# Optimization experiments

Hardware: AMD Instinct MI355X
Metric: run time of the kernel (lower is better)

The kernel has to match this reference:

```python
import jax, jax.numpy as jnp
import numpy as np

MIN_, MAX_, KSZ, IGNORE_IDX = 10, 10, 3, -255
B, H, W = 256, 256, 256
LI_MAX_ITERS = 64


def setup_inputs() -> dict:
    key = jax.random.key(0)
    x = jax.random.uniform(key, (B, 1, H, W), dtype=jnp.float32)
    return {"x": x}


def _otsu(hist):
    # hist: [256] counts. Returns Otsu threshold (bin value); fg = img > t.
    bins = jnp.arange(256, dtype=jnp.float32)
    w0 = jnp.cumsum(hist)[:-1]
    w1 = hist.sum() - w0
    s0 = jnp.cumsum(hist * bins)[:-1]
    s_tot = (hist * bins).sum()
    m0 = s0 / jnp.maximum(w0, 1e-12)
    m1 = (s_tot - s0) / jnp.maximum(w1, 1e-12)
    var_b = w0 * w1 * (m0 - m1) ** 2
    return jnp.argmax(var_b).astype(jnp.float32)


def _li(hist, init_t):
    # Histogram-based Li iterative minimum cross-entropy threshold
    # (skimage.filters.threshold_li with initial_guess=init_t).
    bins = jnp.arange(256, dtype=jnp.float32)
    img_min = jnp.min(jnp.where(hist > 0, bins, 255.0))
    vals = bins - img_min  # shift so values >= 0 (as skimage does)
    csum = jnp.cumsum(hist)
    cvsum = jnp.cumsum(hist * vals)
    n_tot, s_tot = csum[-1], cvsum[-1]
    tol = 0.5  # integer image -> half the minimal value spacing

    def body(state):
        t_curr, _, i = state
        # background: img <= t_curr + img_min
        idx = jnp.clip(jnp.floor(t_curr + img_min).astype(jnp.int32), 0, 255)
        n_back, s_back = csum[idx], cvsum[idx]
        n_fore, s_fore = n_tot - n_back, s_tot - s_back
        mean_back = jnp.where(n_back > 0, s_back / jnp.maximum(n_back, 1.0), 0.0)
        mean_fore = s_fore / jnp.maximum(n_fore, 1.0)
        eps = 1e-12
        t_next = (mean_back - mean_fore) / (
            jnp.log(jnp.maximum(mean_back, eps)) - jnp.log(jnp.maximum(mean_fore, eps)))
        t_next = jnp.where(mean_back < eps, mean_fore / 2.0, t_next)
        return (t_next, t_curr, i + 1)

    def cond(state):
        t_curr, t_prev, i = state
        return (jnp.abs(t_curr - t_prev) > tol) & (i < LI_MAX_ITERS)

    t0 = init_t - img_min
    t_fin, _, _ = jax.lax.while_loop(cond, body, (t0, t0 + 10.0, 0))
    return t_fin + img_min


def _sample_mask(key, region, k):
    # Uniform sampling without replacement of up to k pixels from region
    # (bool [H,W]) via random-score top-k (equiv. to torch.multinomial
    # with uniform probs, w/o replacement).
    flat = region.reshape(-1)
    scores = jnp.where(flat, jax.random.uniform(key, (flat.shape[0],)), -1.0)
    top, idx = jax.lax.top_k(scores, k)
    valid = (top >= 0.0).astype(jnp.int32)
    mask = jnp.zeros(flat.shape[0], jnp.int32).at[idx].max(valid)
    return mask.reshape(region.shape)


def _dilate(m):
    # kornia dilation with ones (KSZ,KSZ) kernel on a 0/1 mask == max filter.
    return jax.lax.reduce_window(m, 0, jax.lax.max, (KSZ, KSZ), (1, 1), "SAME")


def _per_image(img_u8, key_fg, key_bg):
    # img_u8: [H,W] int32 in [0,255]
    hist = jnp.zeros(256, jnp.float32).at[img_u8.ravel()].add(1.0)
    otsu = jnp.clip(_otsu(hist), 1.0, 254.0)  # clamp 0->1, 255->254
    li_t = _li(hist, otsu)
    roi = img_u8.astype(jnp.float32) > li_t

    fg = _sample_mask(key_fg, roi, MAX_)
    bg = _sample_mask(key_bg, jnp.logical_not(roi), MIN_)
    if KSZ > 1:
        fg = _dilate(fg)
        bg = _dilate(bg)

    overlap = (fg + bg) == 2
    fg = jnp.where(overlap, 0, fg)
    bg = jnp.where(overlap, 0, bg)

    seeds = jnp.full((H, W), IGNORE_IDX, jnp.int32)
    seeds = jnp.where(bg == 1, 0, seeds)
    seeds = jnp.where(fg == 1, 1, seeds)
    return seeds


def reference(x):
    b = x.shape[0]
    # (cam*255).astype(uint8): truncation, cam in [0,1]
    img = jnp.clip(jnp.floor(x[:, 0] * 255.0), 0, 255).astype(jnp.int32)
    keys = jax.random.split(jax.random.key(1), (b, 2))
    return jax.vmap(_per_image)(img, keys[:, 0], keys[:, 1])
```

## Files before the change

kernel.cpp:

```cpp
#include <hip/hip_runtime.h>
#include <stdint.h>

#define NPIX 65536
#define IGN (-255)
#define CAP 768
#define HPART 16384
#define SCRI4 4608

__device__ __forceinline__ uint32_t rotl32(uint32_t v, uint32_t r){ return (v<<r)|(v>>(32u-r)); }

__device__ __forceinline__ void tf2x32(uint32_t k0, uint32_t k1, uint32_t x0, uint32_t x1,
                                       uint32_t &o0, uint32_t &o1){
  uint32_t k2 = k0 ^ k1 ^ 0x1BD11BDAu;
  x0 += k0; x1 += k1;
#define TFR(r) { x0 += x1; x1 = rotl32(x1,(r)); x1 ^= x0; }
  TFR(13u) TFR(15u) TFR(26u) TFR(6u)   x0 += k1; x1 += k2 + 1u;
  TFR(17u) TFR(29u) TFR(16u) TFR(24u)  x0 += k2; x1 += k0 + 2u;
  TFR(13u) TFR(15u) TFR(26u) TFR(6u)   x0 += k0; x1 += k1 + 3u;
  TFR(17u) TFR(29u) TFR(16u) TFR(24u)  x0 += k1; x1 += k2 + 4u;
  TFR(13u) TFR(15u) TFR(26u) TFR(6u)   x0 += k2; x1 += k0 + 5u;
#undef TFR
  o0 = x0; o1 = x1;
}

__device__ __forceinline__ unsigned long long packCand(uint32_t bits, uint32_t pix){
  float f = __uint_as_float((bits >> 9) | 0x3f800000u) - 1.0f;
  uint32_t u = __float_as_uint(f) ^ 0x80000000u;
  return ((unsigned long long)u << 32) | (unsigned long long)(0xFFFFFFFFu - pix);
}

__device__ __forceinline__ void t10_insert(unsigned long long* l, unsigned long long c){
  if (c > l[9]) {
    l[9] = c;
#pragma unroll
    for (int i = 9; i > 0; --i){
      unsigned long long a = l[i-1], b2 = l[i];
      if (b2 > a){ l[i-1] = b2; l[i] = a; }
    }
  }
}

__global__ __launch_bounds__(256, 8)
void k1_stream(const float* __restrict__ x, int* __restrict__ out){
  const int blk = blockIdx.x;
  const int b = blk >> 3, j8 = blk & 7;
  const int tid = threadIdx.x;
  const float4* x4 = (const float4*)(x + (size_t)b * NPIX);
  int* base = out + (size_t)b * NPIX;
  int4* o4 = (int4*)base;

  __shared__ uint32_t histR[1024];
#pragma unroll
  for (int k = 0; k < 4; ++k) histR[tid + 256*k] = 0u;
  __syncthreads();

  const int4 f4 = make_int4(IGN, IGN, IGN, IGN);
  const uint32_t c4 = (uint32_t)(tid & 3);
#pragma unroll
  for (int jj = 0; jj < 8; ++jj){
    int i4 = j8*2048 + jj*256 + tid;
    float4 v = x4[i4];
    uint32_t u0 = (uint32_t)min(max((int)floorf(v.x*255.0f),0),255);
    uint32_t u1 = (uint32_t)min(max((int)floorf(v.y*255.0f),0),255);
    uint32_t u2 = (uint32_t)min(max((int)floorf(v.z*255.0f),0),255);
    uint32_t u3 = (uint32_t)min(max((int)floorf(v.w*255.0f),0),255);
    base[i4] = (int)(u0 | (u1<<8) | (u2<<16) | (u3<<24));
    if (i4 >= SCRI4) o4[i4] = f4;
    atomicAdd(&histR[(u0<<2)|c4],1u); atomicAdd(&histR[(u1<<2)|c4],1u);
    atomicAdd(&histR[(u2<<2)|c4],1u); atomicAdd(&histR[(u3<<2)|c4],1u);
  }
  __syncthreads();
  uint32_t s = histR[4*tid] + histR[4*tid+1] + histR[4*tid+2] + histR[4*tid+3];
  base[HPART + j8*256 + tid] = (int)s;
}

__global__ __launch_bounds__(1024, 4)
void k2_final(int* __restrict__ out){
  const int b = blockIdx.x;
  const int tid = threadIdx.x;
  int* meta = out + (size_t)b * NPIX;
  int* outb = meta;

  __shared__ float csum[256], cvsum[256];
  __shared__ int s_qthr, s_nroi;
  __shared__ uint32_t s_kw[4];
  __shared__ unsigned long long buf[2][CAP];
  __shared__ int s_cnt[2], s_fail[2], s_np[2];
  __shared__ unsigned long long s_top[2][64][10];
  __shared__ unsigned long long s_top2[2][8][10];
  __shared__ int s_pr[2][10], s_pc[2][10];

  if (tid < 2){
    uint32_t o0, o1;
    tf2x32(0u, 1u, 0u, (uint32_t)(2*b + tid), o0, o1);
    s_kw[2*tid] = o0; s_kw[2*tid+1] = o1;
    s_cnt[tid] = 0;
  }

  if (tid < 64){
    const int lane = tid;
    int h0 = 0, h1 = 0, h2 = 0, h3 = 0;
    for (int j = 0; j < 8; ++j){
      const int4 p = *(const int4*)&meta[HPART + j*256 + 4*lane];
      h0 += p.x; h1 += p.y; h2 += p.z; h3 += p.w;
    }
    int cand = 256;
    if (h3) cand = 4*lane + 3;
    if (h2) cand = 4*lane + 2;
    if (h1) cand = 4*lane + 1;
    if (h0) cand = 4*lane + 0;
    for (int off = 32; off; off >>= 1) cand = min(cand, __shfl_xor(cand, off));
    const float img_min = (float)cand;
    float c0 = (float)h0, c1 = c0 + h1, c2 = c1 + h2, c3 = c2 + h3;
    float bv = 4.0f*lane - img_min;
    float v0 = h0*bv;
    float v1 = v0 + h1*(bv + 1.0f);
    float v2 = v1 + h2*(bv + 2.0f);
    float v3 = v2 + h3*(bv + 3.0f);
    float cc = c3, vv = v3;
    for (int off = 1; off < 64; off <<= 1){
      float a = __shfl_up(cc, off), b2 = __shfl_up(vv, off);
      if (lane >= off){ cc += a; vv += b2; }
    }
    const float cexc = cc - c3, vexc = vv - v3;
    const float cs0 = cexc+c0, cs1 = cexc+c1, cs2 = cexc+c2, cs3 = cexc+c3;
    const float vs0 = vexc+v0, vs1 = vexc+v1, vs2 = vexc+v2, vs3 = vexc+v3;
    csum[4*lane]   = cs0; csum[4*lane+1]  = cs1;
    csum[4*lane+2] = cs2; csum[4*lane+3]  = cs3;
    cvsum[4*lane]   = vs0; cvsum[4*lane+1] = vs1;
    cvsum[4*lane+2] = vs2; cvsum[4*lane+3] = vs3;
    const float ctot = __shfl(cc, 63), vtot = __shfl(vv, 63);
    const float s_tot_o = vtot + img_min * ctot;
    unsigned long long best = 0ull;
#define OTSU_BIN(CS, VS, J)                                              \
    { int bin = 4*lane + (J);                                            \
      if (bin < 255){                                                    \
        float w0 = (CS);                                                 \
        float w1 = 65536.0f - w0;                                        \
        float cs = (VS) + img_min * (CS);                                \
        float m0 = cs / fmaxf(w0, 1e-12f);                               \
        float m1 = (s_tot_o - cs) / fmaxf(w1, 1e-12f);                   \
        float d = m0 - m1;                                               \
        float vb = (w0*w1) * (d*d);                                      \
        unsigned long long pk =                                          \
          ((unsigned long long)__float_as_uint(vb) << 32) |              \
           (unsigned long long)(255 - bin);                              \
        if (pk > best) best = pk;                                        \
      } }
    OTSU_BIN(cs0, vs0, 0) OTSU_BIN(cs1, vs1, 1)
    OTSU_BIN(cs2, vs2, 2) OTSU_BIN(cs3, vs3, 3)
#undef OTSU_BIN
    for (int off = 32; off; off >>= 1){
      unsigned int hi = (unsigned int)(best >> 32), lo = (unsigned int)best;
      unsigned int hio = (unsigned int)__shfl_xor((int)hi, off);
      unsigned int loo = (unsigned int)__shfl_xor((int)lo, off);
      unsigned long long ob = ((unsigned long long)hio << 32) | loo;
      if (ob > best) best = ob;
    }
    if (lane == 0){
      int bestIdx = 255 - (int)(best & 0xFFFFFFFFull);
      float otsu = fminf(fmaxf((float)bestIdx, 1.0f), 254.0f);
      float n_tot = ctot, s_tot = vtot;
      float t_curr = otsu - img_min, t_prev = t_curr + 10.0f;
      int it = 0;
      while (fabsf(t_curr - t_prev) > 0.5f && it < 64){
        int idx = min(max((int)floorf(t_curr + img_min), 0), 255);
        float n_back = csum[idx], s_back = cvsum[idx];
        float n_fore = n_tot - n_back, s_fore = s_tot - s_back;
        float mean_back = (n_back > 0.0f) ? (s_back / fmaxf(n_back, 1.0f)) : 0.0f;
        float mean_fore = s_fore / fmaxf(n_fore, 1.0f);
        float t_next = (mean_back - mean_fore) /
                       (logf(fmaxf(mean_back, 1e-12f)) - logf(fmaxf(mean_fore, 1e-12f)));
        if (mean_back < 1e-12f) t_next = mean_fore * 0.5f;
        t_prev = t_curr; t_curr = t_next; ++it;
      }
      float lit = t_curr + img_min;
      int qthr;
      if (!(lit == lit)) qthr = 256;
      else               qthr = (int)floorf(lit) + 1;
      s_qthr = qthr;
      int nlo = (qthr <= 0) ? 0 : (int)csum[min(qthr, 256) - 1];
      s_nroi = NPIX - nlo;
    }
  }
  __syncthreads();

  const int qthr = s_qthr;
  const uint32_t fk0 = s_kw[0], fk1 = s_kw[1], bk0 = s_kw[2], bk1 = s_kw[3];
  const int4* u4 = (const int4*)meta;
  for (int k = 0; k < 4; ++k){
    int4 w = u4[tid + 1024*k];
    uint32_t pw0 = (uint32_t)(16*(tid + 1024*k));
#pragma unroll
    for (int m = 0; m < 4; ++m){
      uint32_t pk = (m==0)?(uint32_t)w.x:(m==1)?(uint32_t)w.y:(m==2)?(uint32_t)w.z:(uint32_t)w.w;
      uint32_t pb = pw0 + (uint32_t)(4*m);
#pragma unroll
      for (int s = 0; s < 4; ++s){
        int q = (int)((pk >> (8*s)) & 255u);
        bool r = (q >= qthr);
        uint32_t pix = pb + (uint32_t)s;
        uint32_t o0, o1;
        tf2x32(r ? fk0 : bk0, r ? fk1 : bk1, 0u, pix, o0, o1);
        uint32_t bits = o0 ^ o1;
        if (bits >= 0xFF000000u){
          int r2 = r ? 0 : 1;
          int idx = atomicAdd(&s_cnt[r2], 1);
          if (idx < CAP) buf[r2][idx] = packCand(bits, pix);
        }
      }
    }
  }
  __syncthreads();

  if (tid < 2){
    int rs = tid ? (NPIX - s_nroi) : s_nroi;
    int cc = s_cnt[tid];
    s_fail[tid] = (cc > CAP) || (cc < 10 && cc != rs);
  }
  __syncthreads();

  const int wv = tid >> 6, lane = tid & 63;
  if (wv < 2){
    const int r2 = wv;
    unsigned long long t[10];
#pragma unroll
    for (int i = 0; i < 10; ++i) t[i] = 0ull;
    if (!s_fail[r2]){
      int n = min(s_cnt[r2], CAP);
      for (int i = lane; i < n; i += 64) t10_insert(t, buf[r2][i]);
    } else {
      const uint32_t kk0 = s_kw[2*r2], kk1 = s_kw[2*r2+1];
      for (int k = 0; k < 1024; ++k){
        uint32_t pix = (uint32_t)(lane + 64*k);
        int q = (int)(((uint32_t)meta[pix >> 2] >> (8*(pix & 3u))) & 255u);
        bool r = (q >= qthr);
        if (r == (r2 == 0)){
          uint32_t o0, o1; tf2x32(kk0, kk1, 0u, pix, o0, o1);
          t10_insert(t, packCand(o0 ^ o1, pix));
        }
      }
    }
#pragma unroll
    for (int i = 0; i < 10; ++i) s_top[r2][lane][i] = t[i];
  }
  __syncthreads();
  if (wv < 2 && lane < 8){
    unsigned long long t[10];
#pragma unroll
    for (int i = 0; i < 10; ++i) t[i] = 0ull;
    for (int l2 = 0; l2 < 8; ++l2)
#pragma unroll
      for (int i = 0; i < 10; ++i) t10_insert(t, s_top[wv][lane*8 + l2][i]);
#pragma unroll
    for (int i = 0; i < 10; ++i) s_top2[wv][lane][i] = t[i];
  }
  __syncthreads();
  if (wv < 2 && lane == 0){
    unsigned long long t[10];
#pragma unroll
    for (int i = 0; i < 10; ++i) t[i] = 0ull;
    for (int l2 = 0; l2 < 8; ++l2)
#pragma unroll
      for (int i = 0; i < 10; ++i) t10_insert(t, s_top2[wv][l2][i]);
    int np = 0;
    for (int i = 0; i < 10; ++i){
      if (t[i]){
        uint32_t pix = 0xFFFFFFFFu - (uint32_t)(t[i] & 0xFFFFFFFFull);
        s_pr[wv][np] = (int)(pix >> 8);
        s_pc[wv][np] = (int)(pix & 255u);
        ++np;
      }
    }
    s_np[wv] = np;
  }
  __syncthreads();

  const int4 f4 = make_int4(IGN, IGN, IGN, IGN);
#pragma unroll
  for (int k = 0; k < 5; ++k){
    int idx = tid + 1024*k;
    if (idx < SCRI4) ((int4*)meta)[idx] = f4;
  }
  __syncthreads();

  const int nfg = s_np[0], nbg = s_np[1];
  const int npts = nfg + nbg;
  if (tid < npts*9){
    int k = tid / 9, d = tid - k*9;
    int pr = (k < nfg) ? s_pr[0][k] : s_pr[1][k - nfg];
    int pc = (k < nfg) ? s_pc[0][k] : s_pc[1][k - nfg];
    pr += d/3 - 1; pc += d%3 - 1;
    if (pr >= 0 && pr < 256 && pc >= 0 && pc < 256){
      bool fgd = false, bgd = false;
      for (int i = 0; i < nfg; ++i) fgd |= (abs(pr - s_pr[0][i]) <= 1) && (abs(pc - s_pc[0][i]) <= 1);
      for (int i = 0; i < nbg; ++i) bgd |= (abs(pr - s_pr[1][i]) <= 1) && (abs(pc - s_pc[1][i]) <= 1);
      int val = (fgd && bgd) ? IGN : (fgd ? 1 : 0);
      outb[pr*256 + pc] = val;
    }
  }
}

extern "C" void kernel_launch(void* const* d_in, const int* in_sizes, int n_in,
                              void* d_out, int out_size, void* d_ws, size_t ws_size,
                              hipStream_t stream) {
  const float* x = (const float*)d_in[0];
  int* out = (int*)d_out;
  int B = in_sizes[0] / NPIX;
  k1_stream<<<8*B, 256, 0, stream>>>(x, out);
  k2_final <<<B,  1024, 0, stream>>>(out);
}
```

Measured before the change: 177.7 us.

## Fuse histogram and seed kernels into one per-image block; pair Threefry hashes

```diff
diff --git a/kernel.cpp b/kernel.cpp
--- a/kernel.cpp
+++ b/kernel.cpp
@@ -4,8 +4,6 @@
 #define NPIX 65536
 #define IGN (-255)
 #define CAP 768
-#define HPART 16384
-#define SCRI4 4608
 
 __device__ __forceinline__ uint32_t rotl32(uint32_t v, uint32_t r){ return (v<<r)|(v>>(32u-r)); }
 
@@ -23,6 +21,28 @@
   o0 = x0; o1 = x1;
 }
 
+__device__ __forceinline__ void tf2_pair(uint32_t A0, uint32_t A1, uint32_t xA,
+                                         uint32_t B0, uint32_t B1, uint32_t xB,
+                                         uint32_t &rA, uint32_t &rB){
+  uint32_t A2 = A0 ^ A1 ^ 0x1BD11BDAu;
+  uint32_t B2 = B0 ^ B1 ^ 0x1BD11BDAu;
+  uint32_t a0 = A0, a1 = xA + A1;
+  uint32_t b0 = B0, b1 = xB + B1;
+#define TFR2(r) { a0 += a1; b0 += b1; a1 = rotl32(a1,(r)); b1 = rotl32(b1,(r)); a1 ^= a0; b1 ^= b0; }
+  TFR2(13u) TFR2(15u) TFR2(26u) TFR2(6u)
+  a0 += A1; b0 += B1; a1 += A2 + 1u; b1 += B2 + 1u;
+  TFR2(17u) TFR2(29u) TFR2(16u) TFR2(24u)
+  a0 += A2; b0 += B2; a1 += A0 + 2u; b1 += B0 + 2u;
+  TFR2(13u) TFR2(15u) TFR2(26u) TFR2(6u)
+  a0 += A0; b0 += B0; a1 += A1 + 3u; b1 += B1 + 3u;
+  TFR2(17u) TFR2(29u) TFR2(16u) TFR2(24u)
+  a0 += A1; b0 += B1; a1 += A2 + 4u; b1 += B2 + 4u;
+  TFR2(13u) TFR2(15u) TFR2(26u) TFR2(6u)
+  a0 += A2; b0 += B2; a1 += A0 + 5u; b1 += B0 + 5u;
+#undef TFR2
+  rA = a0 ^ a1; rB = b0 ^ b1;
+}
+
 __device__ __forceinline__ unsigned long long packCand(uint32_t bits, uint32_t pix){
   float f = __uint_as_float((bits >> 9) | 0x3f800000u) - 1.0f;
   uint32_t u = __float_as_uint(f) ^ 0x80000000u;
@@ -40,70 +60,60 @@
   }
 }
 
-__global__ __launch_bounds__(256, 8)
-void k1_stream(const float* __restrict__ x, int* __restrict__ out){
-  const int blk = blockIdx.x;
-  const int b = blk >> 3, j8 = blk & 7;
-  const int tid = threadIdx.x;
-  const float4* x4 = (const float4*)(x + (size_t)b * NPIX);
-  int* base = out + (size_t)b * NPIX;
-  int4* o4 = (int4*)base;
-
-  __shared__ uint32_t histR[1024];
-#pragma unroll
-  for (int k = 0; k < 4; ++k) histR[tid + 256*k] = 0u;
-  __syncthreads();
-
-  const int4 f4 = make_int4(IGN, IGN, IGN, IGN);
-  const uint32_t c4 = (uint32_t)(tid & 3);
-#pragma unroll
-  for (int jj = 0; jj < 8; ++jj){
-    int i4 = j8*2048 + jj*256 + tid;
-    float4 v = x4[i4];
-    uint32_t u0 = (uint32_t)min(max((int)floorf(v.x*255.0f),0),255);
-    uint32_t u1 = (uint32_t)min(max((int)floorf(v.y*255.0f),0),255);
-    uint32_t u2 = (uint32_t)min(max((int)floorf(v.z*255.0f),0),255);
-    uint32_t u3 = (uint32_t)min(max((int)floorf(v.w*255.0f),0),255);
-    base[i4] = (int)(u0 | (u1<<8) | (u2<<16) | (u3<<24));
-    if (i4 >= SCRI4) o4[i4] = f4;
-    atomicAdd(&histR[(u0<<2)|c4],1u); atomicAdd(&histR[(u1<<2)|c4],1u);
-    atomicAdd(&histR[(u2<<2)|c4],1u); atomicAdd(&histR[(u3<<2)|c4],1u);
-  }
-  __syncthreads();
-  uint32_t s = histR[4*tid] + histR[4*tid+1] + histR[4*tid+2] + histR[4*tid+3];
-  base[HPART + j8*256 + tid] = (int)s;
-}
-
-__global__ __launch_bounds__(1024, 4)
-void k2_final(int* __restrict__ out){
+__global__ __launch_bounds__(1024)
+void apm_kernel(const float* __restrict__ x, int* __restrict__ out){
   const int b = blockIdx.x;
   const int tid = threadIdx.x;
-  int* meta = out + (size_t)b * NPIX;
-  int* outb = meta;
-
+  const float* img = x + (size_t)b * NPIX;
+  int* outb = out + (size_t)b * NPIX;
+
+  __shared__ uint32_t histR[1024];
   __shared__ float csum[256], cvsum[256];
-  __shared__ int s_qthr, s_nroi;
   __shared__ uint32_t s_kw[4];
   __shared__ unsigned long long buf[2][CAP];
   __shared__ int s_cnt[2], s_fail[2], s_np[2];
+  __shared__ int s_qthr, s_nroi;
   __shared__ unsigned long long s_top[2][64][10];
   __shared__ unsigned long long s_top2[2][8][10];
   __shared__ int s_pr[2][10], s_pc[2][10];
 
+  histR[tid] = 0u;
   if (tid < 2){
     uint32_t o0, o1;
     tf2x32(0u, 1u, 0u, (uint32_t)(2*b + tid), o0, o1);
     s_kw[2*tid] = o0; s_kw[2*tid+1] = o1;
     s_cnt[tid] = 0;
   }
+  __syncthreads();
+
+  {
+    const float4* x4 = (const float4*)img;
+    int4* o4 = (int4*)outb;
+    const int4 f4 = make_int4(IGN, IGN, IGN, IGN);
+    const uint32_t c4 = (uint32_t)(tid & 3);
+    for (int k = 0; k < 16; ++k){
+      int i4 = tid + 1024*k;
+      float4 v = x4[i4];
+      uint32_t u0 = (uint32_t)min(max((int)floorf(v.x*255.0f),0),255);
+      uint32_t u1 = (uint32_t)min(max((int)floorf(v.y*255.0f),0),255);
+      uint32_t u2 = (uint32_t)min(max((int)floorf(v.z*255.0f),0),255);
+      uint32_t u3 = (uint32_t)min(max((int)floorf(v.w*255.0f),0),255);
+      outb[i4] = (int)(u0 | (u1<<8) | (u2<<16) | (u3<<24));
+      if (i4 >= 4096) o4[i4] = f4;
+      atomicAdd(&histR[(u0<<2)|c4],1u); atomicAdd(&histR[(u1<<2)|c4],1u);
+      atomicAdd(&histR[(u2<<2)|c4],1u); atomicAdd(&histR[(u3<<2)|c4],1u);
+    }
+  }
+  __syncthreads();
 
   if (tid < 64){
     const int lane = tid;
-    int h0 = 0, h1 = 0, h2 = 0, h3 = 0;
-    for (int j = 0; j < 8; ++j){
-      const int4 p = *(const int4*)&meta[HPART + j*256 + 4*lane];
-      h0 += p.x; h1 += p.y; h2 += p.z; h3 += p.w;
-    }
+    const int4* hv = (const int4*)&histR[16*lane];
+    int4 p0 = hv[0], p1 = hv[1], p2 = hv[2], p3 = hv[3];
+    int h0 = p0.x + p0.y + p0.z + p0.w;
+    int h1 = p1.x + p1.y + p1.z + p1.w;
+    int h2 = p2.x + p2.y + p2.z + p2.w;
+    int h3 = p3.x + p3.y + p3.z + p3.w;
     int cand = 256;
     if (h3) cand = 4*lane + 3;
     if (h2) cand = 4*lane + 2;
@@ -135,13 +145,13 @@
 #define OTSU_BIN(CS, VS, J)                                              \
     { int bin = 4*lane + (J);                                            \
       if (bin < 255){                                                    \
-        float w0 = (CS);                                                 \
-        float w1 = 65536.0f - w0;                                        \
+        float w0_ = (CS);                                                \
+        float w1_ = 65536.0f - w0_;                                      \
         float cs = (VS) + img_min * (CS);                                \
-        float m0 = cs / fmaxf(w0, 1e-12f);                               \
-        float m1 = (s_tot_o - cs) / fmaxf(w1, 1e-12f);                   \
+        float m0 = cs / fmaxf(w0_, 1e-12f);                              \
+        float m1 = (s_tot_o - cs) / fmaxf(w1_, 1e-12f);                  \
         float d = m0 - m1;                                               \
-        float vb = (w0*w1) * (d*d);                                      \
+        float vb = (w0_*w1_) * (d*d);                                    \
         unsigned long long pk =                                          \
           ((unsigned long long)__float_as_uint(vb) << 32) |              \
            (unsigned long long)(255 - bin);                              \
@@ -187,7 +197,7 @@
 
   const int qthr = s_qthr;
   const uint32_t fk0 = s_kw[0], fk1 = s_kw[1], bk0 = s_kw[2], bk1 = s_kw[3];
-  const int4* u4 = (const int4*)meta;
+  const int4* u4 = (const int4*)outb;
   for (int k = 0; k < 4; ++k){
     int4 w = u4[tid + 1024*k];
     uint32_t pw0 = (uint32_t)(16*(tid + 1024*k));
@@ -196,17 +206,23 @@
       uint32_t pk = (m==0)?(uint32_t)w.x:(m==1)?(uint32_t)w.y:(m==2)?(uint32_t)w.z:(uint32_t)w.w;
       uint32_t pb = pw0 + (uint32_t)(4*m);
 #pragma unroll
-      for (int s = 0; s < 4; ++s){
-        int q = (int)((pk >> (8*s)) & 255u);
-        bool r = (q >= qthr);
-        uint32_t pix = pb + (uint32_t)s;
-        uint32_t o0, o1;
-        tf2x32(r ? fk0 : bk0, r ? fk1 : bk1, 0u, pix, o0, o1);
-        uint32_t bits = o0 ^ o1;
-        if (bits >= 0xFF000000u){
-          int r2 = r ? 0 : 1;
+      for (int h = 0; h < 2; ++h){
+        int qa = (int)((pk >> (16*h))     & 255u);
+        int qb = (int)((pk >> (16*h + 8)) & 255u);
+        bool ra = (qa >= qthr), rb = (qb >= qthr);
+        uint32_t pixA = pb + (uint32_t)(2*h), pixB = pixA + 1u;
+        uint32_t bitsA, bitsB;
+        tf2_pair(ra ? fk0 : bk0, ra ? fk1 : bk1, pixA,
+                 rb ? fk0 : bk0, rb ? fk1 : bk1, pixB, bitsA, bitsB);
+        if (bitsA >= 0xFF000000u){
+          int r2 = ra ? 0 : 1;
           int idx = atomicAdd(&s_cnt[r2], 1);
-          if (idx < CAP) buf[r2][idx] = packCand(bits, pix);
+          if (idx < CAP) buf[r2][idx] = packCand(bitsA, pixA);
+        }
+        if (bitsB >= 0xFF000000u){
+          int r2 = rb ? 0 : 1;
+          int idx = atomicAdd(&s_cnt[r2], 1);
+          if (idx < CAP) buf[r2][idx] = packCand(bitsB, pixB);
         }
       }
     }
@@ -233,7 +249,7 @@
       const uint32_t kk0 = s_kw[2*r2], kk1 = s_kw[2*r2+1];
       for (int k = 0; k < 1024; ++k){
         uint32_t pix = (uint32_t)(lane + 64*k);
-        int q = (int)(((uint32_t)meta[pix >> 2] >> (8*(pix & 3u))) & 255u);
+        int q = (int)(((uint32_t)outb[pix >> 2] >> (8*(pix & 3u))) & 255u);
         bool r = (q >= qthr);
         if (r == (r2 == 0)){
           uint32_t o0, o1; tf2x32(kk0, kk1, 0u, pix, o0, o1);
@@ -276,11 +292,11 @@
   }
   __syncthreads();
 
-  const int4 f4 = make_int4(IGN, IGN, IGN, IGN);
-#pragma unroll
-  for (int k = 0; k < 5; ++k){
-    int idx = tid + 1024*k;
-    if (idx < SCRI4) ((int4*)meta)[idx] = f4;
+  {
+    int4* o4 = (int4*)outb;
+    const int4 f4 = make_int4(IGN, IGN, IGN, IGN);
+#pragma unroll
+    for (int k = 0; k < 4; ++k) o4[tid + 1024*k] = f4;
   }
   __syncthreads();
 
@@ -307,6 +323,5 @@
   const float* x = (const float*)d_in[0];
   int* out = (int*)d_out;
   int B = in_sizes[0] / NPIX;
-  k1_stream<<<8*B, 256, 0, stream>>>(x, out);
-  k2_final <<<B,  1024, 0, stream>>>(out);
-}
+  apm_kernel<<<B, 1024, 0, stream>>>(x, out);
+}
```

Measured after the change: 172.7 us. -2.8%, faster.
